# Optimization experiments

Measured on AMD Instinct MI355X. Metric: run time of the kernel, lower is better.

The kernel has to match this reference:

```python
import jax, jax.numpy as jnp
import numpy as np

N_NODES = 12288
N_EDGES = 393216
LATENT = 128
EDGE_F = 4


def setup_inputs() -> dict:
    key = jax.random.key(0)
    k1, k2, k3, k4 = jax.random.split(key, 4)
    z = jax.random.normal(k1, (N_NODES, LATENT), dtype=jnp.float32)
    edge_index = jax.random.randint(k2, (2, N_EDGES), 0, N_NODES, dtype=jnp.int64)
    edge_attr = jax.random.normal(k3, (N_EDGES, EDGE_F), dtype=jnp.float32)
    W = jax.random.normal(k4, (1, 2 * LATENT), dtype=jnp.float32) * (1.0 / np.sqrt(2 * LATENT))
    b = jnp.zeros((1,), dtype=jnp.float32)
    return {"z": z, "edge_index": edge_index, "edge_attr": edge_attr, "W": W, "b": b}


def reference(z, edge_index, edge_attr, W, b):
    # z: [N, D], edge_index: [2, E], edge_attr: [E, F], W: [1, 2D], b: [1]
    num_nodes = z.shape[0]
    row, col = edge_index[0], edge_index[1]
    # gather node embeddings per edge and apply tiny linear: [E, 2D] @ [2D, 1]
    edge_features = jnp.concatenate([z[row], z[col]], axis=1)
    specified_edge_probs = (edge_features @ W.T + b)[:, 0]  # [E]
    # scatter edge probs into dense NxN (indexed assignment, like torch)
    full_edge_probs = jnp.zeros((num_nodes, num_nodes), dtype=z.dtype).at[row, col].set(specified_edge_probs)
    # to_dense_adj scatter-adds edge_attr -> [N, N, F]; sum(dim=3) commutes, so add summed attr
    adj = jnp.zeros((num_nodes, num_nodes), dtype=edge_attr.dtype).at[row, col].add(edge_attr.sum(axis=1))
    return adj + full_edge_probs
```

## Files before the change

kernel.cpp:

```cpp
#include <hip/hip_runtime.h>

#define N_NODES 12288
#define N_EDGES 393216
#define LATENT  128
#define BCAP    128
#define ROWS    4
#define RSLOTS  128
#define NBMW    96
#define DOT_BLOCKS (N_NODES / 4)
#define BKT_BLOCKS (N_EDGES / 256)


__global__ void dots_and_bucket(const float* __restrict__ z, const float* __restrict__ W,
                                const int* __restrict__ ei, const float* __restrict__ ea,
                                float* __restrict__ s1, float* __restrict__ s2,
                                unsigned int* __restrict__ cnt,
                                unsigned long long* __restrict__ bpack) {
    if (blockIdx.x < DOT_BLOCKS) {
        int node = (int)(blockIdx.x * 4 + (threadIdx.x >> 6));
        int lane = (int)(threadIdx.x & 63);
        const float* zr = z + (size_t)node * LATENT;
        float a  = zr[lane];
        float bb = zr[lane + 64];
        float p1 = a * W[lane]       + bb * W[lane + 64];
        float p2 = a * W[lane + 128] + bb * W[lane + 192];
        #pragma unroll
        for (int off = 32; off > 0; off >>= 1) {
            p1 += __shfl_down(p1, off, 64);
            p2 += __shfl_down(p2, off, 64);
        }
        if (lane == 0) { s1[node] = p1; s2[node] = p2; }
    } else {
        int e = (int)((blockIdx.x - DOT_BLOCKS) * 256 + threadIdx.x);
        unsigned int r = (unsigned int)ei[e];
        unsigned int c = (unsigned int)ei[e + N_EDGES];
        float4 a4 = ((const float4*)ea)[e];
        float s = a4.x + a4.y + a4.z + a4.w;
        unsigned int pos = atomicAdd(&cnt[r], 1u);
        bpack[(size_t)r * BCAP + pos] =
            ((unsigned long long)c << 32) | (unsigned long long)__float_as_uint(s);
    }
}

__global__ __launch_bounds__(256) void row_fill(const unsigned int* __restrict__ cnt,
                                                const unsigned long long* __restrict__ bpack,
                                                const float* __restrict__ s1,
                                                const float* __restrict__ s2,
                                                const float* __restrict__ bptr,
                                                float* __restrict__ out) {
    __shared__ unsigned int hcol[ROWS][RSLOTS];
    __shared__ float        hval[ROWS][RSLOTS];
    __shared__ unsigned int bm[ROWS][NBMW];
    int r0 = (int)blockIdx.x * ROWS;
    int t  = (int)threadIdx.x;

    float bias = bptr[0];
    float s1r0 = s1[r0], s1r1 = s1[r0 + 1], s1r2 = s1[r0 + 2], s1r3 = s1[r0 + 3];

    for (int i = t; i < ROWS * RSLOTS; i += 256) {
        ((unsigned int*)hcol)[i] = 0u;
        ((float*)hval)[i] = 0.f;
    }
    for (int i = t; i < ROWS * NBMW; i += 256) ((unsigned int*)bm)[i] = 0u;
    __syncthreads();

    #pragma unroll
    for (int rr = 0; rr < ROWS; rr++) {
        int r = r0 + rr;
        unsigned int deg = cnt[r];
        const unsigned long long* seg = bpack + (size_t)r * BCAP;
        for (unsigned int i = (unsigned int)t; i < deg; i += 256u) {
            unsigned long long p = seg[i];
            unsigned int c = (unsigned int)(p >> 32);
            float v = __uint_as_float((unsigned int)p);
            unsigned int h = (c * 2654435761u) >> 25;
            for (;;) {
                unsigned int prev = atomicCAS(&hcol[rr][h], 0u, c + 1u);
                if (prev == 0u) {
                    atomicAdd(&hval[rr][h], v);
                    atomicOr(&bm[rr][c >> 7], 1u << ((c >> 2) & 31));
                    break;
                }
                if (prev == c + 1u) { atomicAdd(&hval[rr][h], v); break; }
                h = (h + 1u) & (RSLOTS - 1u);
            }
        }
    }
    __syncthreads();

    float s1r[ROWS] = {s1r0, s1r1, s1r2, s1r3};

    #pragma unroll
    for (int rr = 0; rr < ROWS; rr++) {
        float4* out4 = (float4*)(out + (size_t)(r0 + rr) * N_NODES);
        #pragma unroll
        for (int i = 0; i < 12; i++) {
            int j = t + i * 256;
            float4 v = make_float4(0.f, 0.f, 0.f, 0.f);
            if (bm[rr][j >> 5] & (1u << (j & 31))) {
                float* vp = (float*)&v;
                #pragma unroll
                for (int k = 0; k < 4; k++) {
                    unsigned int c = ((unsigned int)j << 2) + (unsigned int)k;
                    unsigned int h = (c * 2654435761u) >> 25;
                    for (;;) {
                        unsigned int pc = hcol[rr][h];
                        if (pc == 0u) break;
                        if (pc == c + 1u) {
                            vp[k] = hval[rr][h] + s1r[rr] + s2[c] + bias;
                            break;
                        }
                        h = (h + 1u) & (RSLOTS - 1u);
                    }
                }
            }
            out4[j] = v;
        }
    }
}

extern "C" void kernel_launch(void* const* d_in, const int* in_sizes, int n_in,
                              void* d_out, int out_size, void* d_ws, size_t ws_size,
                              hipStream_t stream) {
    const float* z  = (const float*)d_in[0];
    const int*   ei = (const int*)d_in[1];
    const float* ea = (const float*)d_in[2];
    const float* W  = (const float*)d_in[3];
    const float* b  = (const float*)d_in[4];
    float* out = (float*)d_out;

    char* ws = (char*)d_ws;
    float*              s1    = (float*)(ws + 0);
    float*              s2    = (float*)(ws + 49152);
    unsigned int*       cnt   = (unsigned int*)(ws + 98304);
    unsigned long long* bpack = (unsigned long long*)(ws + 147456);

    hipMemsetAsync(cnt, 0, N_NODES * sizeof(unsigned int), stream);
    dots_and_bucket<<<DOT_BLOCKS + BKT_BLOCKS, 256, 0, stream>>>(z, W, ei, ea, s1, s2, cnt, bpack);
    row_fill<<<N_NODES / ROWS, 256, 0, stream>>>(cnt, bpack, s1, s2, b, out);
}
```

Baseline: 644.1 us.

## Zero-fill output rows unconditionally, then scatter hash entries instead of probing

The occupancy bitmap and the per-column hash probing in the output phase are removed. Each block now streams float4 zeros across its four output rows, issued before the barrier so they can overlap with hash construction. After the barrier, threads walk the occupied hash slots and write only those entries directly. This removes divergent per-element lookups from the store loop, but it depends on barrier ordering so the scattered writes land after the zero stores from other threads.

```diff
diff --git a/kernel.cpp b/kernel.cpp
--- a/kernel.cpp
+++ b/kernel.cpp
@@ -6,7 +6,6 @@
 #define BCAP    128
 #define ROWS    4
 #define RSLOTS  128
-#define NBMW    96
 #define DOT_BLOCKS (N_NODES / 4)
 #define BKT_BLOCKS (N_EDGES / 256)
 
@@ -50,18 +49,17 @@
                                                 float* __restrict__ out) {
     __shared__ unsigned int hcol[ROWS][RSLOTS];
     __shared__ float        hval[ROWS][RSLOTS];
-    __shared__ unsigned int bm[ROWS][NBMW];
+    __shared__ float        s1s[ROWS];
     int r0 = (int)blockIdx.x * ROWS;
     int t  = (int)threadIdx.x;
 
     float bias = bptr[0];
-    float s1r0 = s1[r0], s1r1 = s1[r0 + 1], s1r2 = s1[r0 + 2], s1r3 = s1[r0 + 3];
+    if (t < ROWS) s1s[t] = s1[r0 + t];
 
     for (int i = t; i < ROWS * RSLOTS; i += 256) {
         ((unsigned int*)hcol)[i] = 0u;
         ((float*)hval)[i] = 0.f;
     }
-    for (int i = t; i < ROWS * NBMW; i += 256) ((unsigned int*)bm)[i] = 0u;
     __syncthreads();
 
     #pragma unroll
@@ -76,45 +74,28 @@
             unsigned int h = (c * 2654435761u) >> 25;
             for (;;) {
                 unsigned int prev = atomicCAS(&hcol[rr][h], 0u, c + 1u);
-                if (prev == 0u) {
-                    atomicAdd(&hval[rr][h], v);
-                    atomicOr(&bm[rr][c >> 7], 1u << ((c >> 2) & 31));
-                    break;
-                }
-                if (prev == c + 1u) { atomicAdd(&hval[rr][h], v); break; }
+                if (prev == 0u || prev == c + 1u) { atomicAdd(&hval[rr][h], v); break; }
                 h = (h + 1u) & (RSLOTS - 1u);
             }
         }
     }
+
+    float4* o4 = (float4*)(out + (size_t)r0 * N_NODES);
+    const float4 z4 = make_float4(0.f, 0.f, 0.f, 0.f);
+    #pragma unroll
+    for (int i = 0; i < 48; i++) {
+        o4[t + i * 256] = z4;
+    }
+
     __syncthreads();
 
-    float s1r[ROWS] = {s1r0, s1r1, s1r2, s1r3};
-
-    #pragma unroll
-    for (int rr = 0; rr < ROWS; rr++) {
-        float4* out4 = (float4*)(out + (size_t)(r0 + rr) * N_NODES);
-        #pragma unroll
-        for (int i = 0; i < 12; i++) {
-            int j = t + i * 256;
-            float4 v = make_float4(0.f, 0.f, 0.f, 0.f);
-            if (bm[rr][j >> 5] & (1u << (j & 31))) {
-                float* vp = (float*)&v;
-                #pragma unroll
-                for (int k = 0; k < 4; k++) {
-                    unsigned int c = ((unsigned int)j << 2) + (unsigned int)k;
-                    unsigned int h = (c * 2654435761u) >> 25;
-                    for (;;) {
-                        unsigned int pc = hcol[rr][h];
-                        if (pc == 0u) break;
-                        if (pc == c + 1u) {
-                            vp[k] = hval[rr][h] + s1r[rr] + s2[c] + bias;
-                            break;
-                        }
-                        h = (h + 1u) & (RSLOTS - 1u);
-                    }
-                }
-            }
-            out4[j] = v;
+    for (int sidx = t; sidx < ROWS * RSLOTS; sidx += 256) {
+        int rr = sidx >> 7;
+        int h  = sidx & (RSLOTS - 1);
+        unsigned int pc = hcol[rr][h];
+        if (pc != 0u) {
+            unsigned int c = pc - 1u;
+            out[(size_t)(r0 + rr) * N_NODES + c] = hval[rr][h] + s1s[rr] + s2[c] + bias;
         }
     }
 }
```

Measured after the change: 663.9 us. 1.03x slower.

## Build per-row hash tables in global memory during edge scatter

Applied to the files above, without the earlier changes.

Edges are now inserted directly into per-row open-addressing hash tables in global memory with atomicCAS/atomicAdd, replacing the old per-row bucket arrays and the shared-memory hash build in row_fill. row_fill just copies each row's 128-slot table into shared memory and sets the occupancy bitmap. This drops the bucket write/read pass and the shared-memory atomic build. In exchange it relies on global atomics with possible probe chains, and the memset grows to 12 MB covering both tables.

```diff
diff --git a/kernel.cpp b/kernel.cpp
--- a/kernel.cpp
+++ b/kernel.cpp
@@ -3,7 +3,6 @@
 #define N_NODES 12288
 #define N_EDGES 393216
 #define LATENT  128
-#define BCAP    128
 #define ROWS    4
 #define RSLOTS  128
 #define NBMW    96
@@ -11,11 +10,10 @@
 #define BKT_BLOCKS (N_EDGES / 256)
 
 
-__global__ void dots_and_bucket(const float* __restrict__ z, const float* __restrict__ W,
-                                const int* __restrict__ ei, const float* __restrict__ ea,
-                                float* __restrict__ s1, float* __restrict__ s2,
-                                unsigned int* __restrict__ cnt,
-                                unsigned long long* __restrict__ bpack) {
+__global__ void dots_and_scatter(const float* __restrict__ z, const float* __restrict__ W,
+                                 const int* __restrict__ ei, const float* __restrict__ ea,
+                                 float* __restrict__ s1, float* __restrict__ s2,
+                                 unsigned int* __restrict__ ghcol, float* __restrict__ ghval) {
     if (blockIdx.x < DOT_BLOCKS) {
         int node = (int)(blockIdx.x * 4 + (threadIdx.x >> 6));
         int lane = (int)(threadIdx.x & 63);
@@ -36,14 +34,18 @@
         unsigned int c = (unsigned int)ei[e + N_EDGES];
         float4 a4 = ((const float4*)ea)[e];
         float s = a4.x + a4.y + a4.z + a4.w;
-        unsigned int pos = atomicAdd(&cnt[r], 1u);
-        bpack[(size_t)r * BCAP + pos] =
-            ((unsigned long long)c << 32) | (unsigned long long)__float_as_uint(s);
+        unsigned int base = r * RSLOTS;
+        unsigned int h = (c * 2654435761u) >> 25;
+        for (;;) {
+            unsigned int prev = atomicCAS(&ghcol[base + h], 0u, c + 1u);
+            if (prev == 0u || prev == c + 1u) { atomicAdd(&ghval[base + h], s); break; }
+            h = (h + 1u) & (RSLOTS - 1u);
+        }
     }
 }
 
-__global__ __launch_bounds__(256) void row_fill(const unsigned int* __restrict__ cnt,
-                                                const unsigned long long* __restrict__ bpack,
+__global__ __launch_bounds__(256) void row_fill(const unsigned int* __restrict__ ghcol,
+                                                const float* __restrict__ ghval,
                                                 const float* __restrict__ s1,
                                                 const float* __restrict__ s2,
                                                 const float* __restrict__ bptr,
@@ -57,33 +59,18 @@
     float bias = bptr[0];
     float s1r0 = s1[r0], s1r1 = s1[r0 + 1], s1r2 = s1[r0 + 2], s1r3 = s1[r0 + 3];
 
-    for (int i = t; i < ROWS * RSLOTS; i += 256) {
-        ((unsigned int*)hcol)[i] = 0u;
-        ((float*)hval)[i] = 0.f;
-    }
     for (int i = t; i < ROWS * NBMW; i += 256) ((unsigned int*)bm)[i] = 0u;
     __syncthreads();
 
-    #pragma unroll
-    for (int rr = 0; rr < ROWS; rr++) {
-        int r = r0 + rr;
-        unsigned int deg = cnt[r];
-        const unsigned long long* seg = bpack + (size_t)r * BCAP;
-        for (unsigned int i = (unsigned int)t; i < deg; i += 256u) {
-            unsigned long long p = seg[i];
-            unsigned int c = (unsigned int)(p >> 32);
-            float v = __uint_as_float((unsigned int)p);
-            unsigned int h = (c * 2654435761u) >> 25;
-            for (;;) {
-                unsigned int prev = atomicCAS(&hcol[rr][h], 0u, c + 1u);
-                if (prev == 0u) {
-                    atomicAdd(&hval[rr][h], v);
-                    atomicOr(&bm[rr][c >> 7], 1u << ((c >> 2) & 31));
-                    break;
-                }
-                if (prev == c + 1u) { atomicAdd(&hval[rr][h], v); break; }
-                h = (h + 1u) & (RSLOTS - 1u);
-            }
+    for (int s = t; s < ROWS * RSLOTS; s += 256) {
+        size_t gi = (size_t)r0 * RSLOTS + (size_t)s;
+        unsigned int pc = ghcol[gi];
+        float v = ghval[gi];
+        ((unsigned int*)hcol)[s] = pc;
+        ((float*)hval)[s] = v;
+        if (pc != 0u) {
+            unsigned int c = pc - 1u;
+            atomicOr(&bm[s >> 7][c >> 7], 1u << ((c >> 2) & 31));
         }
     }
     __syncthreads();
@@ -130,12 +117,12 @@
     float* out = (float*)d_out;
 
     char* ws = (char*)d_ws;
-    float*              s1    = (float*)(ws + 0);
-    float*              s2    = (float*)(ws + 49152);
-    unsigned int*       cnt   = (unsigned int*)(ws + 98304);
-    unsigned long long* bpack = (unsigned long long*)(ws + 147456);
+    float*        s1    = (float*)(ws + 0);
+    float*        s2    = (float*)(ws + 49152);
+    unsigned int* ghcol = (unsigned int*)(ws + 98304);
+    float*        ghval = (float*)(ws + 98304 + (size_t)N_NODES * RSLOTS * 4);
 
-    hipMemsetAsync(cnt, 0, N_NODES * sizeof(unsigned int), stream);
-    dots_and_bucket<<<DOT_BLOCKS + BKT_BLOCKS, 256, 0, stream>>>(z, W, ei, ea, s1, s2, cnt, bpack);
-    row_fill<<<N_NODES / ROWS, 256, 0, stream>>>(cnt, bpack, s1, s2, b, out);
+    hipMemsetAsync(ghcol, 0, (size_t)N_NODES * RSLOTS * 8, stream);
+    dots_and_scatter<<<DOT_BLOCKS + BKT_BLOCKS, 256, 0, stream>>>(z, W, ei, ea, s1, s2, ghcol, ghval);
+    row_fill<<<N_NODES / ROWS, 256, 0, stream>>>(ghcol, ghval, s1, s2, b, out);
 }
```

Result: slower. 659.1 us (+2.3%).
